# Optimization experiments

Hardware: AMD Instinct MI355X
Metric: run time of the kernel (lower is better)

Reference implementation:

```python
import jax, jax.numpy as jnp
import numpy as np

N_NODES = 100000
N_EDGES = 3200000
IN_DIM, HD_DIM, OUT_DIM = 512, 256, 128


def spmm(edge_row, edge_col, edge_val, x):
    # y[i] = sum_{e: row[e]=i} val[e] * x[col[e]]  -- sparse adj @ dense x
    msgs = edge_val[:, None] * x[edge_col]          # [E, D]
    return jax.ops.segment_sum(msgs, edge_row, num_segments=N_NODES)


def setup_inputs() -> dict:
    key = jax.random.key(0)
    k1, k2, k3, k4, k5, k6, k7, k8 = jax.random.split(key, 8)
    x = jax.random.normal(k1, (N_NODES, IN_DIM), dtype=jnp.float32)
    edge_row = jax.random.randint(k2, (N_EDGES,), 0, N_NODES, dtype=jnp.int64)
    edge_col = jax.random.randint(k3, (N_EDGES,), 0, N_NODES, dtype=jnp.int64)
    edge_val = jax.random.uniform(k4, (N_EDGES,), dtype=jnp.float32)
    s0 = 1.0 / np.sqrt(IN_DIM)
    s1 = 1.0 / np.sqrt(HD_DIM)
    W0 = jax.random.uniform(k5, (IN_DIM, HD_DIM), dtype=jnp.float32, minval=-s0, maxval=s0)
    b0 = jax.random.uniform(k6, (HD_DIM,), dtype=jnp.float32, minval=-s0, maxval=s0)
    W1 = jax.random.uniform(k7, (HD_DIM, OUT_DIM), dtype=jnp.float32, minval=-s1, maxval=s1)
    b1 = jax.random.uniform(k8, (OUT_DIM,), dtype=jnp.float32, minval=-s1, maxval=s1)
    return {"x": x, "edge_row": edge_row, "edge_col": edge_col, "edge_val": edge_val,
            "W0": W0, "b0": b0, "W1": W1, "b1": b1}


def reference(x, edge_row, edge_col, edge_val, W0, b0, W1, b1):
    # eval mode: dropout is identity
    h = x @ W0 + b0                                  # li0: [N, HD]
    h = spmm(edge_row, edge_col, edge_val, h)        # adj @ h
    h = spmm(edge_row, edge_col, edge_val, h)        # adj @ (adj @ h)
    return jax.nn.relu(h) @ W1 + b1                  # li1(relu(.)): [N, OUT]
```

## Files before the change

kernel.cpp:

```cpp
#include <hip/hip_runtime.h>

#define N_NODES 100000
#define N_EDGES 3200000
#define IN_DIM  512
#define HD_DIM  256
#define OUT_DIM 128

#define NBINS 391
#define EPT   16
#define EPB   (256 * EPT)

typedef short   short8  __attribute__((ext_vector_type(8)));
typedef unsigned short ushort8 __attribute__((ext_vector_type(8)));
typedef float   floatx4 __attribute__((ext_vector_type(4)));

__device__ __forceinline__ unsigned short f2bf(float f) {
    unsigned int u = __float_as_uint(f);
    u += 0x7fffu + ((u >> 16) & 1u);
    return (unsigned short)(u >> 16);
}

__device__ __forceinline__ unsigned f2bf_pk(float lo, float hi) {
    unsigned r;
    asm("v_cvt_pk_bf16_f32 %0, %1, %2" : "=v"(r) : "v"(lo), "v"(hi));
    return r;
}


__global__ __launch_bounds__(256) void bin_count(const int* __restrict__ erow,
                                                 int* __restrict__ gbin, int E) {
    __shared__ int hist[NBINS];
    for (int i = threadIdx.x; i < NBINS; i += 256) hist[i] = 0;
    __syncthreads();
    long base = (long)blockIdx.x * EPB + threadIdx.x * EPT;
    if (base < E) {
        const int4* p = (const int4*)(erow + base);
#pragma unroll
        for (int v = 0; v < 4; v++) {
            int4 r4 = p[v];
            atomicAdd(&hist[r4.x >> 8], 1);
            atomicAdd(&hist[r4.y >> 8], 1);
            atomicAdd(&hist[r4.z >> 8], 1);
            atomicAdd(&hist[r4.w >> 8], 1);
        }
    }
    __syncthreads();
    for (int i = threadIdx.x; i < NBINS; i += 256)
        if (hist[i]) atomicAdd(&gbin[i], hist[i]);
}

__global__ void bin_scan(const int* __restrict__ gbin, int* __restrict__ bin_base,
                         int* __restrict__ gcursor, int* __restrict__ rowptr) {
    __shared__ int sd[512];
    int v = (threadIdx.x < NBINS) ? gbin[threadIdx.x] : 0;
    sd[threadIdx.x] = v;
    __syncthreads();
    for (int off = 1; off < 512; off <<= 1) {
        int add = (threadIdx.x >= off) ? sd[threadIdx.x - off] : 0;
        __syncthreads();
        sd[threadIdx.x] += add;
        __syncthreads();
    }
    if (threadIdx.x < NBINS) {
        int ex = sd[threadIdx.x] - v;
        bin_base[threadIdx.x] = ex;
        gcursor[threadIdx.x] = ex;
    }
    if (threadIdx.x == 0) { bin_base[NBINS] = N_EDGES; rowptr[N_NODES] = N_EDGES; }
}

__global__ __launch_bounds__(256) void bin_scatter(const int* __restrict__ erow,
                                                   const int* __restrict__ ecol,
                                                   const float* __restrict__ eval,
                                                   int* __restrict__ gcursor,
                                                   uint2* __restrict__ binned, int E) {
    __shared__ int hist[NBINS];
    __shared__ int cur[NBINS];
    for (int i = threadIdx.x; i < NBINS; i += 256) hist[i] = 0;
    __syncthreads();
    long base = (long)blockIdx.x * EPB + threadIdx.x * EPT;
    int rows[EPT];
    const bool valid = base < E;
    if (valid) {
        const int4* p = (const int4*)(erow + base);
#pragma unroll
        for (int v = 0; v < 4; v++) {
            int4 r = p[v];
            rows[4 * v + 0] = r.x; rows[4 * v + 1] = r.y;
            rows[4 * v + 2] = r.z; rows[4 * v + 3] = r.w;
        }
#pragma unroll
        for (int u = 0; u < EPT; u++) atomicAdd(&hist[rows[u] >> 8], 1);
    }
    __syncthreads();
    for (int i = threadIdx.x; i < NBINS; i += 256) {
        int h = hist[i];
        cur[i] = h ? atomicAdd(&gcursor[i], h) : 0;
    }
    __syncthreads();
    if (valid) {
        const int4*   pc = (const int4*)(ecol + base);
        const float4* pv = (const float4*)(eval + base);
#pragma unroll
        for (int v = 0; v < 4; v++) {
            int4 c4 = pc[v];
            float4 v4 = pv[v];
            int   cs[4] = {c4.x, c4.y, c4.z, c4.w};
            float vs[4] = {v4.x, v4.y, v4.z, v4.w};
#pragma unroll
            for (int u = 0; u < 4; u++) {
                int r = rows[4 * v + u];
                int pos = atomicAdd(&cur[r >> 8], 1);
                binned[pos] = make_uint2(((unsigned)(r & 255) << 20) | (unsigned)cs[u],
                                         __float_as_uint(vs[u]));
            }
        }
    }
}

__global__ __launch_bounds__(256) void bin_finalize(const int* __restrict__ bin_base,
                                                    const uint2* __restrict__ binned,
                                                    int* __restrict__ rowptr,
                                                    uint2* __restrict__ csr) {
    __shared__ int hist[256];
    __shared__ int cur[256];
    const int b = blockIdx.x;
    const int s = bin_base[b], e = bin_base[b + 1];
    const int t = threadIdx.x;
    hist[t] = 0;
    __syncthreads();
    for (int i = s + t; i < e; i += 256)
        atomicAdd(&hist[binned[i].x >> 20], 1);
    __syncthreads();
    int v = hist[t];
    for (int off = 1; off < 256; off <<= 1) {
        int add = (t >= off) ? hist[t - off] : 0;
        __syncthreads();
        hist[t] += add;
        __syncthreads();
    }
    int excl = hist[t] - v;
    int r = (b << 8) + t;
    if (r < N_NODES) rowptr[r] = s + excl;
    cur[t] = s + excl;
    __syncthreads();
    for (int i = s + t; i < e; i += 256) {
        uint2 ev = binned[i];
        int pos = atomicAdd(&cur[ev.x >> 20], 1);
        csr[pos] = make_uint2(ev.x & 0xFFFFFu, ev.y);
    }
}


__global__ void transpose_bf16(const float* __restrict__ in, unsigned short* __restrict__ out,
                               int K, int N) {
    int idx = blockIdx.x * blockDim.x + threadIdx.x;
    if (idx < K * N) {
        int k = idx / N, n = idx - k * N;
        out[n * K + k] = f2bf(in[idx]);
    }
}


template <bool A_FP32, bool RELU_A, bool OUT_BF16, int BN>
__global__ __launch_bounds__(256, 2) void gemm_mfma(const void* __restrict__ Av,
                                                    const unsigned short* __restrict__ BT,
                                                    const float* __restrict__ bias,
                                                    void* __restrict__ Cv,
                                                    int M, int N, int K) {
    constexpr int NJ = BN / 32;
    __shared__ unsigned short As[128 * 40];
    __shared__ unsigned short Bs[BN * 40];
    const int tid  = threadIdx.x;
    const int lane = tid & 63;
    const int wv   = tid >> 6;
    const int wm   = (wv >> 1) * 64;
    const int wn   = (wv & 1) * (BN / 2);
    const int mrow = lane & 15;
    const int q    = lane >> 4;
    const int bm   = blockIdx.x * 128;
    const int bn   = blockIdx.y * BN;

    floatx4 acc[4][NJ] = {};

    const int srow = tid >> 1;
    const int skh  = (tid & 1) * 16;

    for (int k0 = 0; k0 < K; k0 += 32) {
        {
            const int grow = bm + srow;
            if (A_FP32) {
                uint4 w0, w1;
                if (grow < M) {
                    const float* A = (const float*)Av;
                    const float4* p = (const float4*)&A[(long)grow * K + k0 + skh];
                    float4 f;
                    f = p[0]; w0.x = f2bf_pk(f.x, f.y); w0.y = f2bf_pk(f.z, f.w);
                    f = p[1]; w0.z = f2bf_pk(f.x, f.y); w0.w = f2bf_pk(f.z, f.w);
                    f = p[2]; w1.x = f2bf_pk(f.x, f.y); w1.y = f2bf_pk(f.z, f.w);
                    f = p[3]; w1.z = f2bf_pk(f.x, f.y); w1.w = f2bf_pk(f.z, f.w);
                } else {
                    w0 = make_uint4(0, 0, 0, 0);
                    w1 = make_uint4(0, 0, 0, 0);
                }
                *(uint4*)&As[srow * 40 + skh]     = w0;
                *(uint4*)&As[srow * 40 + skh + 8] = w1;
            } else {
                unsigned short tmp[16];
                const unsigned short* A = (const unsigned short*)Av;
                if (grow < M) {
                    const ushort8* p = (const ushort8*)&A[(long)grow * K + k0 + skh];
                    ushort8 u0 = p[0], u1 = p[1];
#pragma unroll
                    for (int v = 0; v < 8; v++) { tmp[v] = u0[v]; tmp[8 + v] = u1[v]; }
                    if (RELU_A) {
#pragma unroll
                        for (int v = 0; v < 16; v++)
                            if (tmp[v] & 0x8000u) tmp[v] = 0;
                    }
                } else {
#pragma unroll
                    for (int v = 0; v < 16; v++) tmp[v] = 0;
                }
                ushort8* dst = (ushort8*)&As[srow * 40 + skh];
                ushort8 w0, w1;
#pragma unroll
                for (int v = 0; v < 8; v++) { w0[v] = tmp[v]; w1[v] = tmp[8 + v]; }
                dst[0] = w0;
                dst[1] = w1;
            }
        }
        if (BN == 128) {
            const int gn = bn + srow;
            const ushort8* p = (const ushort8*)&BT[(long)gn * K + k0 + skh];
            ushort8* dst = (ushort8*)&Bs[srow * 40 + skh];
            dst[0] = p[0];
            dst[1] = p[1];
        } else {
            const int gn = bn + tid;
            const ushort8* p = (const ushort8*)&BT[(long)gn * K + k0];
            ushort8* dst = (ushort8*)&Bs[tid * 40];
            dst[0] = p[0];
            dst[1] = p[1];
            dst[2] = p[2];
            dst[3] = p[3];
        }
        __syncthreads();

        short8 af[4], bf[NJ];
#pragma unroll
        for (int i = 0; i < 4; i++)
            af[i] = *(const short8*)&As[(wm + i * 16 + mrow) * 40 + q * 8];
#pragma unroll
        for (int j = 0; j < NJ; j++)
            bf[j] = *(const short8*)&Bs[(wn + j * 16 + mrow) * 40 + q * 8];
#pragma unroll
        for (int i = 0; i < 4; i++)
#pragma unroll
            for (int j = 0; j < NJ; j++)
                acc[i][j] = __builtin_amdgcn_mfma_f32_16x16x32_bf16(af[i], bf[j], acc[i][j], 0, 0, 0);
        __syncthreads();
    }

#pragma unroll
    for (int i = 0; i < 4; i++) {
#pragma unroll
        for (int r = 0; r < 4; r++) {
            const int row = bm + wm + i * 16 + q * 4 + r;
            if (row < M) {
#pragma unroll
                for (int j = 0; j < NJ; j++) {
                    const int col = bn + wn + j * 16 + mrow;
                    float v = acc[i][j][r] + bias[col];
                    if (OUT_BF16)
                        ((unsigned short*)Cv)[(long)row * N + col] = f2bf(v);
                    else
                        ((float*)Cv)[(long)row * N + col] = v;
                }
            }
        }
    }
}


__global__ __launch_bounds__(256) void spmm_bf16(const int* __restrict__ rowptr,
                                                 const uint2* __restrict__ edges,
                                                 const unsigned short* __restrict__ Hin,
                                                 unsigned short* __restrict__ Hout) {
    const int wave = threadIdx.x >> 6;
    const int lane = threadIdx.x & 63;
    const int r = blockIdx.x * 4 + wave;
    if (r >= N_NODES) return;
    const int s = rowptr[r];
    const int e = rowptr[r + 1];
    const uint2* __restrict__ Hv = (const uint2*)Hin;
    float a0 = 0.f, a1 = 0.f, a2 = 0.f, a3 = 0.f;

    for (int base = s; base < e; base += 64) {
        int idx = base + lane;
        uint2 ev = (idx < e) ? edges[idx] : make_uint2(0u, 0u);
        int cnt = e - base;
        if (cnt > 64) cnt = 64;
        for (int j0 = 0; j0 < cnt; j0 += 8) {
            uint2 h[8];
            float v[8];
#pragma unroll
            for (int u = 0; u < 8; u++) {
                int   c = __shfl((int)ev.x, j0 + u);
                v[u]    = __uint_as_float((unsigned)__shfl((int)ev.y, j0 + u));
                h[u]    = Hv[((unsigned)c << 6) + lane];
            }
#pragma unroll
            for (int u = 0; u < 8; u++) {
                a0 += v[u] * __uint_as_float(h[u].x << 16);
                a1 += v[u] * __uint_as_float(h[u].x & 0xffff0000u);
                a2 += v[u] * __uint_as_float(h[u].y << 16);
                a3 += v[u] * __uint_as_float(h[u].y & 0xffff0000u);
            }
        }
    }
    uint2 o;
    o.x = (unsigned)f2bf(a0) | ((unsigned)f2bf(a1) << 16);
    o.y = (unsigned)f2bf(a2) | ((unsigned)f2bf(a3) << 16);
    ((uint2*)Hout)[((unsigned)r << 6) + lane] = o;
}


extern "C" void kernel_launch(void* const* d_in, const int* in_sizes, int n_in,
                              void* d_out, int out_size, void* d_ws, size_t ws_size,
                              hipStream_t stream) {
    const float* x    = (const float*)d_in[0];
    const int*   erow = (const int*)d_in[1];
    const int*   ecol = (const int*)d_in[2];
    const float* eval = (const float*)d_in[3];
    const float* W0   = (const float*)d_in[4];
    const float* b0   = (const float*)d_in[5];
    const float* W1   = (const float*)d_in[6];
    const float* b1   = (const float*)d_in[7];
    float* out = (float*)d_out;

    char* ws = (char*)d_ws;
    size_t off = 0;
    auto alloc = [&](size_t bytes) {
        void* p = ws + off;
        off += (bytes + 255) & ~(size_t)255;
        return p;
    };
    int*            rowptr   = (int*)alloc((N_NODES + 1) * sizeof(int));
    int*            gbin     = (int*)alloc(NBINS * sizeof(int));
    int*            gcursor  = (int*)alloc(NBINS * sizeof(int));
    int*            bin_base = (int*)alloc((NBINS + 1) * sizeof(int));
    uint2*          binned   = (uint2*)alloc((size_t)N_EDGES * sizeof(uint2));
    uint2*          csr      = (uint2*)alloc((size_t)N_EDGES * sizeof(uint2));
    unsigned short* W0T      = (unsigned short*)alloc((size_t)IN_DIM * HD_DIM * sizeof(unsigned short));
    unsigned short* W1T      = (unsigned short*)alloc((size_t)HD_DIM * OUT_DIM * sizeof(unsigned short));
    unsigned short* Ha       = (unsigned short*)alloc((size_t)N_NODES * HD_DIM * sizeof(unsigned short));
    unsigned short* Hb       = (unsigned short*)alloc((size_t)N_NODES * HD_DIM * sizeof(unsigned short));

    const int nblk = (N_EDGES + EPB - 1) / EPB;

    hipMemsetAsync(gbin, 0, NBINS * sizeof(int), stream);
    bin_count<<<nblk, 256, 0, stream>>>(erow, gbin, N_EDGES);
    bin_scan<<<1, 512, 0, stream>>>(gbin, bin_base, gcursor, rowptr);
    bin_scatter<<<nblk, 256, 0, stream>>>(erow, ecol, eval, gcursor, binned, N_EDGES);
    bin_finalize<<<NBINS, 256, 0, stream>>>(bin_base, binned, rowptr, csr);

    transpose_bf16<<<(IN_DIM * HD_DIM + 255) / 256, 256, 0, stream>>>(W0, W0T, IN_DIM, HD_DIM);
    transpose_bf16<<<(HD_DIM * OUT_DIM + 255) / 256, 256, 0, stream>>>(W1, W1T, HD_DIM, OUT_DIM);

    gemm_mfma<true, false, true, 256><<<dim3((N_NODES + 127) / 128, HD_DIM / 256), 256, 0, stream>>>(
        x, W0T, b0, Ha, N_NODES, HD_DIM, IN_DIM);

    spmm_bf16<<<(N_NODES + 3) / 4, 256, 0, stream>>>(rowptr, csr, Ha, Hb);
    spmm_bf16<<<(N_NODES + 3) / 4, 256, 0, stream>>>(rowptr, csr, Hb, Ha);

    gemm_mfma<false, true, false, 128><<<dim3((N_NODES + 127) / 128, OUT_DIM / 128), 256, 0, stream>>>(
        Ha, W1T, b1, out, N_NODES, OUT_DIM, HD_DIM);
}
```

Baseline: 896.1 us.

## Build CSR with fixed-capacity bins and LDS-staged coalesced scatters

Removes the separate bin_count and bin_scan passes. Each bin now gets a fixed region of BINCAP slots, so bin_scatter can reserve space with an atomic on a per-bin counter and needs no prior global prefix sum. bin_scatter and bin_finalize first sort edges in LDS and then write them out contiguously, which replaces scattered global writes with coalesced ones. In exchange the spmm end-of-row lookup needs a binend array, LDS use grows (lower occupancy), and any edges beyond BINCAP in a bin are silently dropped. That is only safe because the random row indices spread edges roughly evenly across bins.

```diff
diff --git a/kernel.cpp b/kernel.cpp
--- a/kernel.cpp
+++ b/kernel.cpp
@@ -6,9 +6,10 @@
 #define HD_DIM  256
 #define OUT_DIM 128
 
-#define NBINS 391
-#define EPT   16
-#define EPB   (256 * EPT)
+#define NBINS  391
+#define BINCAP 9216
+#define EPT    16
+#define EPB    (256 * EPT)
 
 typedef short   short8  __attribute__((ext_vector_type(8)));
 typedef unsigned short ushort8 __attribute__((ext_vector_type(8)));
@@ -27,58 +28,24 @@
 }
 
 
-__global__ __launch_bounds__(256) void bin_count(const int* __restrict__ erow,
-                                                 int* __restrict__ gbin, int E) {
-    __shared__ int hist[NBINS];
-    for (int i = threadIdx.x; i < NBINS; i += 256) hist[i] = 0;
-    __syncthreads();
-    long base = (long)blockIdx.x * EPB + threadIdx.x * EPT;
-    if (base < E) {
-        const int4* p = (const int4*)(erow + base);
-#pragma unroll
-        for (int v = 0; v < 4; v++) {
-            int4 r4 = p[v];
-            atomicAdd(&hist[r4.x >> 8], 1);
-            atomicAdd(&hist[r4.y >> 8], 1);
-            atomicAdd(&hist[r4.z >> 8], 1);
-            atomicAdd(&hist[r4.w >> 8], 1);
-        }
-    }
-    __syncthreads();
-    for (int i = threadIdx.x; i < NBINS; i += 256)
-        if (hist[i]) atomicAdd(&gbin[i], hist[i]);
-}
-
-__global__ void bin_scan(const int* __restrict__ gbin, int* __restrict__ bin_base,
-                         int* __restrict__ gcursor, int* __restrict__ rowptr) {
-    __shared__ int sd[512];
-    int v = (threadIdx.x < NBINS) ? gbin[threadIdx.x] : 0;
-    sd[threadIdx.x] = v;
-    __syncthreads();
-    for (int off = 1; off < 512; off <<= 1) {
-        int add = (threadIdx.x >= off) ? sd[threadIdx.x - off] : 0;
-        __syncthreads();
-        sd[threadIdx.x] += add;
-        __syncthreads();
-    }
-    if (threadIdx.x < NBINS) {
-        int ex = sd[threadIdx.x] - v;
-        bin_base[threadIdx.x] = ex;
-        gcursor[threadIdx.x] = ex;
-    }
-    if (threadIdx.x == 0) { bin_base[NBINS] = N_EDGES; rowptr[N_NODES] = N_EDGES; }
-}
-
 __global__ __launch_bounds__(256) void bin_scatter(const int* __restrict__ erow,
                                                    const int* __restrict__ ecol,
                                                    const float* __restrict__ eval,
-                                                   int* __restrict__ gcursor,
+                                                   int* __restrict__ gcnt,
                                                    uint2* __restrict__ binned, int E) {
     __shared__ int hist[NBINS];
+    __shared__ int sd[512];
+    __shared__ int lbase[NBINS];
+    __shared__ int gbase[NBINS];
     __shared__ int cur[NBINS];
-    for (int i = threadIdx.x; i < NBINS; i += 256) hist[i] = 0;
-    __syncthreads();
-    long base = (long)blockIdx.x * EPB + threadIdx.x * EPT;
+    __shared__ unsigned short sbin[EPB];
+    __shared__ uint2 sedge[EPB];
+
+    const int t = threadIdx.x;
+    for (int i = t; i < NBINS; i += 256) hist[i] = 0;
+    __syncthreads();
+
+    long base = (long)blockIdx.x * EPB + t * EPT;
     int rows[EPT];
     const bool valid = base < E;
     if (valid) {
@@ -93,11 +60,28 @@
         for (int u = 0; u < EPT; u++) atomicAdd(&hist[rows[u] >> 8], 1);
     }
     __syncthreads();
-    for (int i = threadIdx.x; i < NBINS; i += 256) {
-        int h = hist[i];
-        cur[i] = h ? atomicAdd(&gcursor[i], h) : 0;
-    }
-    __syncthreads();
+
+    sd[t]       = (t < NBINS) ? hist[t] : 0;
+    sd[t + 256] = (t + 256 < NBINS) ? hist[t + 256] : 0;
+    __syncthreads();
+    for (int off = 1; off < 512; off <<= 1) {
+        int a0 = (t >= off) ? sd[t - off] : 0;
+        int a1 = (t + 256 >= off) ? sd[t + 256 - off] : 0;
+        __syncthreads();
+        sd[t] += a0;
+        sd[t + 256] += a1;
+        __syncthreads();
+    }
+
+    for (int i = t; i < NBINS; i += 256) {
+        int h  = hist[i];
+        int lb = sd[i] - h;
+        lbase[i] = lb;
+        cur[i]   = lb;
+        gbase[i] = h ? (i * BINCAP + atomicAdd(&gcnt[i], h)) : 0;
+    }
+    __syncthreads();
+
     if (valid) {
         const int4*   pc = (const int4*)(ecol + base);
         const float4* pv = (const float4*)(eval + base);
@@ -110,26 +94,42 @@
 #pragma unroll
             for (int u = 0; u < 4; u++) {
                 int r = rows[4 * v + u];
-                int pos = atomicAdd(&cur[r >> 8], 1);
-                binned[pos] = make_uint2(((unsigned)(r & 255) << 20) | (unsigned)cs[u],
+                int bin = r >> 8;
+                int lpos = atomicAdd(&cur[bin], 1);
+                sedge[lpos] = make_uint2(((unsigned)(r & 255) << 20) | (unsigned)cs[u],
                                          __float_as_uint(vs[u]));
-            }
-        }
-    }
-}
-
-__global__ __launch_bounds__(256) void bin_finalize(const int* __restrict__ bin_base,
+                sbin[lpos] = (unsigned short)bin;
+            }
+        }
+    }
+    __syncthreads();
+
+    const int ns = sd[NBINS - 1];
+    for (int i = t; i < ns; i += 256) {
+        int bin = sbin[i];
+        int gpos = gbase[bin] + (i - lbase[bin]);
+        if (gpos < (bin + 1) * BINCAP)
+            binned[gpos] = sedge[i];
+    }
+}
+
+__global__ __launch_bounds__(256) void bin_finalize(const int* __restrict__ gcnt,
                                                     const uint2* __restrict__ binned,
                                                     int* __restrict__ rowptr,
+                                                    int* __restrict__ binend,
                                                     uint2* __restrict__ csr) {
     __shared__ int hist[256];
     __shared__ int cur[256];
+    __shared__ uint2 stage[BINCAP];
     const int b = blockIdx.x;
-    const int s = bin_base[b], e = bin_base[b + 1];
     const int t = threadIdx.x;
+    int n = gcnt[b];
+    if (n > BINCAP) n = BINCAP;
+    const int s = b * BINCAP;
+
     hist[t] = 0;
     __syncthreads();
-    for (int i = s + t; i < e; i += 256)
+    for (int i = s + t; i < s + n; i += 256)
         atomicAdd(&hist[binned[i].x >> 20], 1);
     __syncthreads();
     int v = hist[t];
@@ -141,14 +141,18 @@
     }
     int excl = hist[t] - v;
     int r = (b << 8) + t;
-    if (r < N_NODES) rowptr[r] = s + excl;
-    cur[t] = s + excl;
-    __syncthreads();
-    for (int i = s + t; i < e; i += 256) {
+    if (r <= N_NODES) rowptr[r] = s + excl;
+    if (t == 0) binend[b] = s + n;
+    cur[t] = excl;
+    __syncthreads();
+    for (int i = s + t; i < s + n; i += 256) {
         uint2 ev = binned[i];
         int pos = atomicAdd(&cur[ev.x >> 20], 1);
-        csr[pos] = make_uint2(ev.x & 0xFFFFFu, ev.y);
-    }
+        stage[pos] = make_uint2(ev.x & 0xFFFFFu, ev.y);
+    }
+    __syncthreads();
+    for (int i = t; i < n; i += 256)
+        csr[s + i] = stage[i];
 }
 
 
@@ -284,6 +288,7 @@
 
 
 __global__ __launch_bounds__(256) void spmm_bf16(const int* __restrict__ rowptr,
+                                                 const int* __restrict__ binend,
                                                  const uint2* __restrict__ edges,
                                                  const unsigned short* __restrict__ Hin,
                                                  unsigned short* __restrict__ Hout) {
@@ -292,7 +297,7 @@
     const int r = blockIdx.x * 4 + wave;
     if (r >= N_NODES) return;
     const int s = rowptr[r];
-    const int e = rowptr[r + 1];
+    const int e = ((r & 255) == 255) ? binend[r >> 8] : rowptr[r + 1];
     const uint2* __restrict__ Hv = (const uint2*)Hin;
     float a0 = 0.f, a1 = 0.f, a2 = 0.f, a3 = 0.f;
 
@@ -347,11 +352,10 @@
         return p;
     };
     int*            rowptr   = (int*)alloc((N_NODES + 1) * sizeof(int));
-    int*            gbin     = (int*)alloc(NBINS * sizeof(int));
-    int*            gcursor  = (int*)alloc(NBINS * sizeof(int));
-    int*            bin_base = (int*)alloc((NBINS + 1) * sizeof(int));
-    uint2*          binned   = (uint2*)alloc((size_t)N_EDGES * sizeof(uint2));
-    uint2*          csr      = (uint2*)alloc((size_t)N_EDGES * sizeof(uint2));
+    int*            gcnt     = (int*)alloc(NBINS * sizeof(int));
+    int*            binend   = (int*)alloc(NBINS * sizeof(int));
+    uint2*          binned   = (uint2*)alloc((size_t)NBINS * BINCAP * sizeof(uint2));
+    uint2*          csr      = (uint2*)alloc((size_t)NBINS * BINCAP * sizeof(uint2));
     unsigned short* W0T      = (unsigned short*)alloc((size_t)IN_DIM * HD_DIM * sizeof(unsigned short));
     unsigned short* W1T      = (unsigned short*)alloc((size_t)HD_DIM * OUT_DIM * sizeof(unsigned short));
     unsigned short* Ha       = (unsigned short*)alloc((size_t)N_NODES * HD_DIM * sizeof(unsigned short));
@@ -359,11 +363,9 @@
 
     const int nblk = (N_EDGES + EPB - 1) / EPB;
 
-    hipMemsetAsync(gbin, 0, NBINS * sizeof(int), stream);
-    bin_count<<<nblk, 256, 0, stream>>>(erow, gbin, N_EDGES);
-    bin_scan<<<1, 512, 0, stream>>>(gbin, bin_base, gcursor, rowptr);
-    bin_scatter<<<nblk, 256, 0, stream>>>(erow, ecol, eval, gcursor, binned, N_EDGES);
-    bin_finalize<<<NBINS, 256, 0, stream>>>(bin_base, binned, rowptr, csr);
+    hipMemsetAsync(gcnt, 0, NBINS * sizeof(int), stream);
+    bin_scatter<<<nblk, 256, 0, stream>>>(erow, ecol, eval, gcnt, binned, N_EDGES);
+    bin_finalize<<<NBINS, 256, 0, stream>>>(gcnt, binned, rowptr, binend, csr);
 
     transpose_bf16<<<(IN_DIM * HD_DIM + 255) / 256, 256, 0, stream>>>(W0, W0T, IN_DIM, HD_DIM);
     transpose_bf16<<<(HD_DIM * OUT_DIM + 255) / 256, 256, 0, stream>>>(W1, W1T, HD_DIM, OUT_DIM);
@@ -371,8 +373,8 @@
     gemm_mfma<true, false, true, 256><<<dim3((N_NODES + 127) / 128, HD_DIM / 256), 256, 0, stream>>>(
         x, W0T, b0, Ha, N_NODES, HD_DIM, IN_DIM);
 
-    spmm_bf16<<<(N_NODES + 3) / 4, 256, 0, stream>>>(rowptr, csr, Ha, Hb);
-    spmm_bf16<<<(N_NODES + 3) / 4, 256, 0, stream>>>(rowptr, csr, Hb, Ha);
+    spmm_bf16<<<(N_NODES + 3) / 4, 256, 0, stream>>>(rowptr, binend, csr, Ha, Hb);
+    spmm_bf16<<<(N_NODES + 3) / 4, 256, 0, stream>>>(rowptr, binend, csr, Hb, Ha);
 
     gemm_mfma<false, true, false, 128><<<dim3((N_NODES + 127) / 128, OUT_DIM / 128), 256, 0, stream>>>(
         Ha, W1T, b1, out, N_NODES, OUT_DIM, HD_DIM);
```

After: 861.8 us. -3.8%, faster.

## Build CSR with per-row global atomics and nontemporal SpMM edge/output access

Applied to the files above, without the earlier changes.

Replaces the two-level bin sort (bin histogram, bin scatter, per-bin finalize) with a direct per-row count in global atomics, a two-level prefix scan, and a single scatter that uses per-row global atomic cursors. This drops the intermediate binned edge buffer and one full pass over the edges. The two weight transposes are merged into one launch, and SpMM uses nontemporal loads for edges and nontemporal stores for outputs to reduce cache pollution. In exchange, edge order within a row becomes nondeterministic, and global atomic contention and scattered writes may cost more than the LDS-based binning did.

```diff
diff --git a/kernel.cpp b/kernel.cpp
--- a/kernel.cpp
+++ b/kernel.cpp
@@ -27,137 +27,110 @@
 }
 
 
-__global__ __launch_bounds__(256) void bin_count(const int* __restrict__ erow,
-                                                 int* __restrict__ gbin, int E) {
-    __shared__ int hist[NBINS];
-    for (int i = threadIdx.x; i < NBINS; i += 256) hist[i] = 0;
-    __syncthreads();
+__global__ __launch_bounds__(256) void row_count(const int* __restrict__ erow,
+                                                 int* __restrict__ rowcnt, int E) {
     long base = (long)blockIdx.x * EPB + threadIdx.x * EPT;
     if (base < E) {
         const int4* p = (const int4*)(erow + base);
 #pragma unroll
         for (int v = 0; v < 4; v++) {
             int4 r4 = p[v];
-            atomicAdd(&hist[r4.x >> 8], 1);
-            atomicAdd(&hist[r4.y >> 8], 1);
-            atomicAdd(&hist[r4.z >> 8], 1);
-            atomicAdd(&hist[r4.w >> 8], 1);
-        }
-    }
+            atomicAdd(&rowcnt[r4.x], 1);
+            atomicAdd(&rowcnt[r4.y], 1);
+            atomicAdd(&rowcnt[r4.z], 1);
+            atomicAdd(&rowcnt[r4.w], 1);
+        }
+    }
+}
+
+__global__ __launch_bounds__(256) void scan_local(const int* __restrict__ rowcnt,
+                                                  int* __restrict__ locex,
+                                                  int* __restrict__ binsum) {
+    __shared__ int sd[256];
+    const int b = blockIdx.x, t = threadIdx.x;
+    const int r = (b << 8) + t;
+    int v = (r < N_NODES) ? rowcnt[r] : 0;
+    sd[t] = v;
     __syncthreads();
-    for (int i = threadIdx.x; i < NBINS; i += 256)
-        if (hist[i]) atomicAdd(&gbin[i], hist[i]);
-}
-
-__global__ void bin_scan(const int* __restrict__ gbin, int* __restrict__ bin_base,
-                         int* __restrict__ gcursor, int* __restrict__ rowptr) {
+    for (int off = 1; off < 256; off <<= 1) {
+        int add = (t >= off) ? sd[t - off] : 0;
+        __syncthreads();
+        sd[t] += add;
+        __syncthreads();
+    }
+    if (r < N_NODES) locex[r] = sd[t] - v;
+    if (t == 255) binsum[b] = sd[255];
+}
+
+__global__ void scan_bins(const int* __restrict__ binsum, int* __restrict__ binbase,
+                          int* __restrict__ rowptr) {
     __shared__ int sd[512];
-    int v = (threadIdx.x < NBINS) ? gbin[threadIdx.x] : 0;
-    sd[threadIdx.x] = v;
+    const int t = threadIdx.x;
+    int v = (t < NBINS) ? binsum[t] : 0;
+    sd[t] = v;
     __syncthreads();
     for (int off = 1; off < 512; off <<= 1) {
-        int add = (threadIdx.x >= off) ? sd[threadIdx.x - off] : 0;
-        __syncthreads();
-        sd[threadIdx.x] += add;
-        __syncthreads();
-    }
-    if (threadIdx.x < NBINS) {
-        int ex = sd[threadIdx.x] - v;
-        bin_base[threadIdx.x] = ex;
-        gcursor[threadIdx.x] = ex;
-    }
-    if (threadIdx.x == 0) { bin_base[NBINS] = N_EDGES; rowptr[N_NODES] = N_EDGES; }
-}
-
-__global__ __launch_bounds__(256) void bin_scatter(const int* __restrict__ erow,
+        int add = (t >= off) ? sd[t - off] : 0;
+        __syncthreads();
+        sd[t] += add;
+        __syncthreads();
+    }
+    if (t < NBINS) binbase[t] = sd[t] - v;
+    if (t == 0) rowptr[N_NODES] = N_EDGES;
+}
+
+__global__ __launch_bounds__(256) void finalize_ptr(const int* __restrict__ binbase,
+                                                    const int* __restrict__ locex,
+                                                    int* __restrict__ rowptr,
+                                                    int* __restrict__ cursor) {
+    const int r = (blockIdx.x << 8) + threadIdx.x;
+    if (r < N_NODES) {
+        int p = binbase[r >> 8] + locex[r];
+        rowptr[r] = p;
+        cursor[r] = p;
+    }
+}
+
+__global__ __launch_bounds__(256) void row_scatter(const int* __restrict__ erow,
                                                    const int* __restrict__ ecol,
                                                    const float* __restrict__ eval,
-                                                   int* __restrict__ gcursor,
-                                                   uint2* __restrict__ binned, int E) {
-    __shared__ int hist[NBINS];
-    __shared__ int cur[NBINS];
-    for (int i = threadIdx.x; i < NBINS; i += 256) hist[i] = 0;
-    __syncthreads();
+                                                   int* __restrict__ cursor,
+                                                   uint2* __restrict__ csr, int E) {
     long base = (long)blockIdx.x * EPB + threadIdx.x * EPT;
-    int rows[EPT];
-    const bool valid = base < E;
-    if (valid) {
-        const int4* p = (const int4*)(erow + base);
-#pragma unroll
-        for (int v = 0; v < 4; v++) {
-            int4 r = p[v];
-            rows[4 * v + 0] = r.x; rows[4 * v + 1] = r.y;
-            rows[4 * v + 2] = r.z; rows[4 * v + 3] = r.w;
-        }
-#pragma unroll
-        for (int u = 0; u < EPT; u++) atomicAdd(&hist[rows[u] >> 8], 1);
-    }
-    __syncthreads();
-    for (int i = threadIdx.x; i < NBINS; i += 256) {
-        int h = hist[i];
-        cur[i] = h ? atomicAdd(&gcursor[i], h) : 0;
-    }
-    __syncthreads();
-    if (valid) {
+    if (base < E) {
+        const int4*   pr = (const int4*)(erow + base);
         const int4*   pc = (const int4*)(ecol + base);
         const float4* pv = (const float4*)(eval + base);
 #pragma unroll
         for (int v = 0; v < 4; v++) {
-            int4 c4 = pc[v];
+            int4   r4 = pr[v];
+            int4   c4 = pc[v];
             float4 v4 = pv[v];
+            int   rs[4] = {r4.x, r4.y, r4.z, r4.w};
             int   cs[4] = {c4.x, c4.y, c4.z, c4.w};
             float vs[4] = {v4.x, v4.y, v4.z, v4.w};
 #pragma unroll
             for (int u = 0; u < 4; u++) {
-                int r = rows[4 * v + u];
-                int pos = atomicAdd(&cur[r >> 8], 1);
-                binned[pos] = make_uint2(((unsigned)(r & 255) << 20) | (unsigned)cs[u],
-                                         __float_as_uint(vs[u]));
-            }
-        }
-    }
-}
-
-__global__ __launch_bounds__(256) void bin_finalize(const int* __restrict__ bin_base,
-                                                    const uint2* __restrict__ binned,
-                                                    int* __restrict__ rowptr,
-                                                    uint2* __restrict__ csr) {
-    __shared__ int hist[256];
-    __shared__ int cur[256];
-    const int b = blockIdx.x;
-    const int s = bin_base[b], e = bin_base[b + 1];
-    const int t = threadIdx.x;
-    hist[t] = 0;
-    __syncthreads();
-    for (int i = s + t; i < e; i += 256)
-        atomicAdd(&hist[binned[i].x >> 20], 1);
-    __syncthreads();
-    int v = hist[t];
-    for (int off = 1; off < 256; off <<= 1) {
-        int add = (t >= off) ? hist[t - off] : 0;
-        __syncthreads();
-        hist[t] += add;
-        __syncthreads();
-    }
-    int excl = hist[t] - v;
-    int r = (b << 8) + t;
-    if (r < N_NODES) rowptr[r] = s + excl;
-    cur[t] = s + excl;
-    __syncthreads();
-    for (int i = s + t; i < e; i += 256) {
-        uint2 ev = binned[i];
-        int pos = atomicAdd(&cur[ev.x >> 20], 1);
-        csr[pos] = make_uint2(ev.x & 0xFFFFFu, ev.y);
-    }
-}
-
-
-__global__ void transpose_bf16(const float* __restrict__ in, unsigned short* __restrict__ out,
-                               int K, int N) {
+                int pos = atomicAdd(&cursor[rs[u]], 1);
+                csr[pos] = make_uint2((unsigned)cs[u], __float_as_uint(vs[u]));
+            }
+        }
+    }
+}
+
+
+__global__ void transpose_w(const float* __restrict__ W0, unsigned short* __restrict__ W0T,
+                            const float* __restrict__ W1, unsigned short* __restrict__ W1T) {
     int idx = blockIdx.x * blockDim.x + threadIdx.x;
-    if (idx < K * N) {
-        int k = idx / N, n = idx - k * N;
-        out[n * K + k] = f2bf(in[idx]);
+    if (idx < IN_DIM * HD_DIM) {
+        int k = idx / HD_DIM, n = idx - k * HD_DIM;
+        W0T[n * IN_DIM + k] = f2bf(W0[idx]);
+    } else {
+        int j = idx - IN_DIM * HD_DIM;
+        if (j < HD_DIM * OUT_DIM) {
+            int k = j / OUT_DIM, n = j - k * OUT_DIM;
+            W1T[n * HD_DIM + k] = f2bf(W1[j]);
+        }
     }
 }
 
@@ -298,7 +271,13 @@
 
     for (int base = s; base < e; base += 64) {
         int idx = base + lane;
-        uint2 ev = (idx < e) ? edges[idx] : make_uint2(0u, 0u);
+        uint2 ev = make_uint2(0u, 0u);
+        if (idx < e) {
+            unsigned long long raw =
+                __builtin_nontemporal_load((const unsigned long long*)edges + idx);
+            ev.x = (unsigned)raw;
+            ev.y = (unsigned)(raw >> 32);
+        }
         int cnt = e - base;
         if (cnt > 64) cnt = 64;
         for (int j0 = 0; j0 < cnt; j0 += 8) {
@@ -319,10 +298,9 @@
             }
         }
     }
-    uint2 o;
-    o.x = (unsigned)f2bf(a0) | ((unsigned)f2bf(a1) << 16);
-    o.y = (unsigned)f2bf(a2) | ((unsigned)f2bf(a3) << 16);
-    ((uint2*)Hout)[((unsigned)r << 6) + lane] = o;
+    unsigned long long o = (unsigned long long)((unsigned)f2bf(a0) | ((unsigned)f2bf(a1) << 16))
+                         | ((unsigned long long)((unsigned)f2bf(a2) | ((unsigned)f2bf(a3) << 16)) << 32);
+    __builtin_nontemporal_store(o, (unsigned long long*)Hout + (((unsigned)r << 6) + lane));
 }
 
 
@@ -347,10 +325,11 @@
         return p;
     };
     int*            rowptr   = (int*)alloc((N_NODES + 1) * sizeof(int));
-    int*            gbin     = (int*)alloc(NBINS * sizeof(int));
-    int*            gcursor  = (int*)alloc(NBINS * sizeof(int));
-    int*            bin_base = (int*)alloc((NBINS + 1) * sizeof(int));
-    uint2*          binned   = (uint2*)alloc((size_t)N_EDGES * sizeof(uint2));
+    int*            rowcnt   = (int*)alloc(N_NODES * sizeof(int));
+    int*            locex    = (int*)alloc(N_NODES * sizeof(int));
+    int*            cursor   = (int*)alloc(N_NODES * sizeof(int));
+    int*            binsum   = (int*)alloc(NBINS * sizeof(int));
+    int*            binbase  = (int*)alloc(NBINS * sizeof(int));
     uint2*          csr      = (uint2*)alloc((size_t)N_EDGES * sizeof(uint2));
     unsigned short* W0T      = (unsigned short*)alloc((size_t)IN_DIM * HD_DIM * sizeof(unsigned short));
     unsigned short* W1T      = (unsigned short*)alloc((size_t)HD_DIM * OUT_DIM * sizeof(unsigned short));
@@ -359,14 +338,15 @@
 
     const int nblk = (N_EDGES + EPB - 1) / EPB;
 
-    hipMemsetAsync(gbin, 0, NBINS * sizeof(int), stream);
-    bin_count<<<nblk, 256, 0, stream>>>(erow, gbin, N_EDGES);
-    bin_scan<<<1, 512, 0, stream>>>(gbin, bin_base, gcursor, rowptr);
-    bin_scatter<<<nblk, 256, 0, stream>>>(erow, ecol, eval, gcursor, binned, N_EDGES);
-    bin_finalize<<<NBINS, 256, 0, stream>>>(bin_base, binned, rowptr, csr);
-
-    transpose_bf16<<<(IN_DIM * HD_DIM + 255) / 256, 256, 0, stream>>>(W0, W0T, IN_DIM, HD_DIM);
-    transpose_bf16<<<(HD_DIM * OUT_DIM + 255) / 256, 256, 0, stream>>>(W1, W1T, HD_DIM, OUT_DIM);
+    hipMemsetAsync(rowcnt, 0, N_NODES * sizeof(int), stream);
+    row_count<<<nblk, 256, 0, stream>>>(erow, rowcnt, N_EDGES);
+    scan_local<<<NBINS, 256, 0, stream>>>(rowcnt, locex, binsum);
+    scan_bins<<<1, 512, 0, stream>>>(binsum, binbase, rowptr);
+    finalize_ptr<<<NBINS, 256, 0, stream>>>(binbase, locex, rowptr, cursor);
+    row_scatter<<<nblk, 256, 0, stream>>>(erow, ecol, eval, cursor, csr, N_EDGES);
+
+    transpose_w<<<(IN_DIM * HD_DIM + HD_DIM * OUT_DIM + 255) / 256, 256, 0, stream>>>(
+        W0, W0T, W1, W1T);
 
     gemm_mfma<true, false, true, 256><<<dim3((N_NODES + 127) / 128, HD_DIM / 256), 256, 0, stream>>>(
         x, W0T, b0, Ha, N_NODES, HD_DIM, IN_DIM);
```

After: 1.201 ms. 1.34x slower.
